# Performance work log

Measured on AMD Instinct MI355X. Metric: run time of the kernel, lower is better.

The kernel has to match this reference:

```python
import jax, jax.numpy as jnp
import numpy as np

DIM = 512
HEADS = 8
SCALE = (DIM / HEADS) ** (-0.5)  # = head_dim^-0.5


def setup_inputs() -> dict:
    key = jax.random.key(0)
    kq, kk, kv = jax.random.split(key, 3)
    B, N, D = 4, 2048, DIM
    return {
        "Q": jax.random.normal(kq, (B, N, D), dtype=jnp.float32),
        "K": jax.random.normal(kk, (B, N, D), dtype=jnp.float32),
        "V": jax.random.normal(kv, (B, N, D), dtype=jnp.float32),
    }


def _split_heads(x):
    b, n, hd = x.shape
    d = hd // HEADS
    return x.reshape(b, n, HEADS, d).transpose(0, 2, 1, 3)  # [b,h,n,d]


def reference(Q, K, V):
    q = _split_heads(Q)
    k = _split_heads(K)
    v = _split_heads(V)
    dots = jnp.einsum('bhid,bhjd->bhij', q, k) * SCALE
    attn = jax.nn.softmax(dots, axis=-1)
    out = jnp.einsum('bhij,bhjd->bhid', attn, v)
    b, h, n, d = out.shape
    return out.transpose(0, 2, 1, 3).reshape(b, n, h * d)
```

## Files before the change

### kernel.cpp

```cpp
#include <hip/hip_runtime.h>

typedef _Float16 half4 __attribute__((ext_vector_type(4)));
typedef _Float16 half8 __attribute__((ext_vector_type(8)));
typedef float floatx4 __attribute__((ext_vector_type(4)));

constexpr int NSEQ = 2048;
constexpr int NDIM = 512;
constexpr int DH   = 64;
constexpr float SCALE = 0.125f;
constexpr float SCALE_L2E = 0.125f * 1.44269504088896340736f;

constexpr int KB9 = 32;
constexpr int NT9 = NSEQ / KB9;
constexpr int KB = 64;
constexpr int NT = NSEQ / KB;

#if __has_builtin(__builtin_amdgcn_exp2f)
__device__ __forceinline__ float fast_exp2(float x) { return __builtin_amdgcn_exp2f(x); }
#else
__device__ __forceinline__ float fast_exp2(float x) {
    float r; asm("v_exp_f32 %0, %1\n\ts_nop 1" : "=v"(r) : "v"(x)); return r;
}
#endif

__global__ __launch_bounds__(256) void mha_prep9(const float* __restrict__ K,
                                                 const float* __restrict__ V,
                                                 _Float16* __restrict__ Kh,
                                                 _Float16* __restrict__ Vh)
{
    const int bid = blockIdx.x;
    const int isV = bid >> 11;
    const int t   = bid & 2047;
    const int kt  = t & 63, bh = t >> 6;
    const int h = bh & 7, b = bh >> 3;
    const int n0 = kt * KB9;
    _Float16* dst = (isV ? Vh : Kh) + (size_t)(bh * 64 + kt) * 2048;

    const int tid = threadIdx.x;
    const int f = tid >> 6, l = tid & 63, lr = l & 15, lg = l >> 4;
    half8 w;
    if (!isV) {
        const int row = n0 + (f >> 1) * 16 + lr;
        const int c0  = (f & 1) * 32 + lg * 8;
        const float* src = K + ((size_t)b * NSEQ + row) * NDIM + h * DH + c0;
        floatx4 x0 = *(const floatx4*)src;
        floatx4 x1 = *(const floatx4*)(src + 4);
        #pragma unroll
        for (int j = 0; j < 4; ++j) { w[j] = (_Float16)x0[j]; w[4 + j] = (_Float16)x1[j]; }
    } else {
        const int d  = f * 16 + lr;
        const int k0 = lg * 4;
        const float* src = V + ((size_t)(b * NSEQ + n0 + k0)) * NDIM + h * DH + d;
        #pragma unroll
        for (int j = 0; j < 4; ++j) {
            w[j]     = (_Float16)src[(size_t)j * NDIM];
            w[4 + j] = (_Float16)src[(size_t)(16 + j) * NDIM];
        }
    }
    *(half8*)(dst + (size_t)tid * 8) = w;
}

__launch_bounds__(256, 3)
__global__ void mha_fwd13(const float* __restrict__ Q,
                          const _Float16* __restrict__ Kh,
                          const _Float16* __restrict__ Vh,
                          float* __restrict__ O)
{
    __shared__ float mrg[2][34][64];

    const int tid = threadIdx.x, wave = tid >> 6, lane = tid & 63;
    const int qgrp = wave & 1, khalf = wave >> 1;
    const int lr = lane & 15, lg = lane >> 4;

    const int bid = blockIdx.x;
    const int bh  = (bid & 7) + 8 * (bid >> 8);
    const int qw  = (bid >> 3) & 31;
    const int h = bh & 7, b = bh >> 3;
    const int qrow0 = qw * 64 + qgrp * 32;

    half8 aq[2][2];
    #pragma unroll
    for (int qs = 0; qs < 2; ++qs) {
        const float* qp = Q + ((size_t)b * NSEQ + qrow0 + qs * 16 + lr) * NDIM + h * DH;
        #pragma unroll
        for (int c = 0; c < 2; ++c) {
            floatx4 x0 = *(const floatx4*)(qp + c * 32 + lg * 8);
            floatx4 x1 = *(const floatx4*)(qp + c * 32 + lg * 8 + 4);
            #pragma unroll
            for (int j = 0; j < 4; ++j) {
                aq[qs][c][j]     = (_Float16)(x0[j] * SCALE_L2E);
                aq[qs][c][4 + j] = (_Float16)(x1[j] * SCALE_L2E);
            }
        }
    }

    const char* kbase = (const char*)Kh + (size_t)bh * 64 * 4096 + lane * 16;
    const char* vbase = (const char*)Vh + (size_t)bh * 64 * 4096 + lane * 16;

    floatx4 accT[4][2];
    floatx4 accL[2];
    #pragma unroll
    for (int dt = 0; dt < 4; ++dt)
        #pragma unroll
        for (int qs = 0; qs < 2; ++qs) accT[dt][qs] = (floatx4){0.f, 0.f, 0.f, 0.f};
    #pragma unroll
    for (int qs = 0; qs < 2; ++qs) accL[qs] = (floatx4){0.f, 0.f, 0.f, 0.f};
    const half8 ones8 = {(_Float16)1.f, (_Float16)1.f, (_Float16)1.f, (_Float16)1.f,
                         (_Float16)1.f, (_Float16)1.f, (_Float16)1.f, (_Float16)1.f};

    half8 kA[4], kB[4];

    const int kt0 = khalf * (NT9 / 2);
    const int ktL = kt0 + NT9 / 2 - 1;

    auto LK = [&](int kt, half8* d) {
        const char* p = kbase + (size_t)kt * 4096;
        d[0] = *(const half8*)(p);
        d[1] = *(const half8*)(p + 1024);
        d[2] = *(const half8*)(p + 2048);
        d[3] = *(const half8*)(p + 3072);
    };

    auto BODY = [&](int kt, half8* kC, half8* kN) {
        const char* vp = vbase + (size_t)kt * 4096;
        half8 vf0 = *(const half8*)(vp);
        half8 vf1 = *(const half8*)(vp + 1024);
        half8 vf2 = *(const half8*)(vp + 2048);
        half8 vf3 = *(const half8*)(vp + 3072);
        const int ktn = (kt < ktL) ? kt + 1 : kt;
        LK(ktn, kN);

        #pragma unroll
        for (int qs = 0; qs < 2; ++qs) {
            floatx4 s0 = (floatx4){0.f, 0.f, 0.f, 0.f};
            s0 = __builtin_amdgcn_mfma_f32_16x16x32_f16(kC[0], aq[qs][0], s0, 0, 0, 0);
            s0 = __builtin_amdgcn_mfma_f32_16x16x32_f16(kC[1], aq[qs][1], s0, 0, 0, 0);
            floatx4 s1 = (floatx4){0.f, 0.f, 0.f, 0.f};
            s1 = __builtin_amdgcn_mfma_f32_16x16x32_f16(kC[2], aq[qs][0], s1, 0, 0, 0);
            s1 = __builtin_amdgcn_mfma_f32_16x16x32_f16(kC[3], aq[qs][1], s1, 0, 0, 0);

            union { unsigned int u[4]; half8 h; } pw;
            {
                const float e0 = fast_exp2(s0[0]);
                const float e1 = fast_exp2(s0[1]);
                const float e2 = fast_exp2(s0[2]);
                const float e3 = fast_exp2(s0[3]);
                pw.u[0] = __builtin_bit_cast(unsigned int, __builtin_amdgcn_cvt_pkrtz(e0, e1));
                pw.u[1] = __builtin_bit_cast(unsigned int, __builtin_amdgcn_cvt_pkrtz(e2, e3));
            }
            {
                const float e0 = fast_exp2(s1[0]);
                const float e1 = fast_exp2(s1[1]);
                const float e2 = fast_exp2(s1[2]);
                const float e3 = fast_exp2(s1[3]);
                pw.u[2] = __builtin_bit_cast(unsigned int, __builtin_amdgcn_cvt_pkrtz(e0, e1));
                pw.u[3] = __builtin_bit_cast(unsigned int, __builtin_amdgcn_cvt_pkrtz(e2, e3));
            }
            const half8 pb8 = pw.h;

            __builtin_amdgcn_s_setprio(1);
            accL[qs] = __builtin_amdgcn_mfma_f32_16x16x32_f16(ones8, pb8, accL[qs], 0, 0, 0);
            accT[0][qs] = __builtin_amdgcn_mfma_f32_16x16x32_f16(vf0, pb8, accT[0][qs], 0, 0, 0);
            accT[1][qs] = __builtin_amdgcn_mfma_f32_16x16x32_f16(vf1, pb8, accT[1][qs], 0, 0, 0);
            accT[2][qs] = __builtin_amdgcn_mfma_f32_16x16x32_f16(vf2, pb8, accT[2][qs], 0, 0, 0);
            accT[3][qs] = __builtin_amdgcn_mfma_f32_16x16x32_f16(vf3, pb8, accT[3][qs], 0, 0, 0);
            __builtin_amdgcn_s_setprio(0);
        }
    };

    LK(kt0, kA);
    for (int it = 0; it < NT9 / 2; it += 2) {
        BODY(kt0 + it,     kA, kB);
        BODY(kt0 + it + 1, kB, kA);
    }

    __syncthreads();
    if (khalf == 1) {
        float (*m)[64] = mrg[qgrp];
        #pragma unroll
        for (int dt = 0; dt < 4; ++dt)
            #pragma unroll
            for (int qs = 0; qs < 2; ++qs)
                #pragma unroll
                for (int r = 0; r < 4; ++r)
                    m[dt * 8 + qs * 4 + r][lane] = accT[dt][qs][r];
        #pragma unroll
        for (int qs = 0; qs < 2; ++qs) m[32 + qs][lane] = accL[qs][0];
    }
    __syncthreads();
    if (khalf == 0) {
        float (*m)[64] = mrg[qgrp];
        #pragma unroll
        for (int qs = 0; qs < 2; ++qs) {
            const float inv = 1.0f / (accL[qs][0] + m[32 + qs][lane]);
            float* op = O + ((size_t)b * NSEQ + qrow0 + qs * 16 + lr) * NDIM + h * DH;
            #pragma unroll
            for (int dt = 0; dt < 4; ++dt) {
                floatx4 o;
                #pragma unroll
                for (int r = 0; r < 4; ++r)
                    o[r] = (accT[dt][qs][r] + m[dt * 8 + qs * 4 + r][lane]) * inv;
                *(floatx4*)(op + dt * 16 + lg * 4) = o;
            }
        }
    }
}

constexpr int QB2 = 64;
constexpr int LDK = DH + 8;
constexpr int LDV = KB + 8;

__launch_bounds__(256, 4)
__global__ void mha_fwd2(const float* __restrict__ Q,
                         const float* __restrict__ K,
                         const float* __restrict__ V,
                         float* __restrict__ O)
{
    __shared__ _Float16 sK[2][KB * LDK];
    __shared__ _Float16 sVT[2][DH * LDV];

    const int tid = threadIdx.x, wave = tid >> 6, lane = tid & 63;
    const int lr = lane & 15, lg = lane >> 4;
    const int bid = blockIdx.x;
    const int qt = bid & 31, bh = bid >> 5;
    const int h = bh & 7, b = bh >> 3;
    const int qrow0 = qt * QB2 + wave * 16;

    half8 aq[2];
    {
        const float* qp = Q + ((size_t)b * NSEQ + qrow0 + lr) * NDIM + h * DH;
        #pragma unroll
        for (int c = 0; c < 2; ++c) {
            floatx4 x0 = *(const floatx4*)(qp + c * 32 + lg * 8);
            floatx4 x1 = *(const floatx4*)(qp + c * 32 + lg * 8 + 4);
            #pragma unroll
            for (int j = 0; j < 4; ++j) {
                aq[c][j] = (_Float16)(x0[j] * SCALE);
                aq[c][4 + j] = (_Float16)(x1[j] * SCALE);
            }
        }
    }
    const int jk = tid >> 2, ck = (tid & 3) * 16;
    const int jv = (tid & 15) * 4, cv = (tid >> 4) * 4;
    const float* kbase = K + (size_t)b * NSEQ * NDIM + h * DH;
    const float* vbase = V + (size_t)b * NSEQ * NDIM + h * DH;

    floatx4 rk[4], rv[4];
    auto LOAD = [&](int kt) {
        const float* ks = kbase + (size_t)(kt * KB + jk) * NDIM + ck;
        #pragma unroll
        for (int q4 = 0; q4 < 4; ++q4) rk[q4] = *(const floatx4*)(ks + q4 * 4);
        const float* vs = vbase + (size_t)(kt * KB + jv) * NDIM + cv;
        #pragma unroll
        for (int i = 0; i < 4; ++i) rv[i] = *(const floatx4*)(vs + (size_t)i * NDIM);
    };
    auto WRITE = [&](int buf) {
        #pragma unroll
        for (int q4 = 0; q4 < 4; ++q4) {
            half4 w = { (_Float16)rk[q4][0], (_Float16)rk[q4][1],
                        (_Float16)rk[q4][2], (_Float16)rk[q4][3] };
            *(half4*)&sK[buf][jk * LDK + ck + q4 * 4] = w;
        }
        #pragma unroll
        for (int cc = 0; cc < 4; ++cc) {
            half4 w = { (_Float16)rv[0][cc], (_Float16)rv[1][cc],
                        (_Float16)rv[2][cc], (_Float16)rv[3][cc] };
            *(half4*)&sVT[buf][(cv + cc) * LDV + jv] = w;
        }
    };

    floatx4 accT[4];
    #pragma unroll
    for (int t = 0; t < 4; ++t) accT[t] = (floatx4){0.f, 0.f, 0.f, 0.f};
    float m_run = -1e30f, l_run = 0.f;

    LOAD(0);
    #pragma unroll 2
    for (int kt = 0; kt < NT; ++kt) {
        const int buf = kt & 1;
        WRITE(buf);
        if (kt + 1 < NT) LOAD(kt + 1);
        __syncthreads();

        floatx4 s[4];
        #pragma unroll
        for (int t = 0; t < 4; ++t) {
            half8 bk0 = *(const half8*)&sK[buf][(t * 16 + lr) * LDK + lg * 8];
            half8 bk1 = *(const half8*)&sK[buf][(t * 16 + lr) * LDK + 32 + lg * 8];
            floatx4 z = (floatx4){0.f, 0.f, 0.f, 0.f};
            z = __builtin_amdgcn_mfma_f32_16x16x32_f16(bk0, aq[0], z, 0, 0, 0);
            z = __builtin_amdgcn_mfma_f32_16x16x32_f16(bk1, aq[1], z, 0, 0, 0);
            s[t] = z;
        }
        float lm = s[0][0];
        #pragma unroll
        for (int t = 0; t < 4; ++t)
            #pragma unroll
            for (int r = 0; r < 4; ++r) lm = fmaxf(lm, s[t][r]);
        lm = fmaxf(lm, __shfl_xor(lm, 16, 64));
        lm = fmaxf(lm, __shfl_xor(lm, 32, 64));
        const float mn = fmaxf(m_run, lm);
        const float f = __expf(m_run - mn);
        m_run = mn;
        #pragma unroll
        for (int t = 0; t < 4; ++t)
            #pragma unroll
            for (int r = 0; r < 4; ++r) s[t][r] = __expf(s[t][r] - mn);
        float ls = 0.f;
        #pragma unroll
        for (int t = 0; t < 4; ++t) ls += (s[t][0] + s[t][1]) + (s[t][2] + s[t][3]);
        ls += __shfl_xor(ls, 16, 64);
        ls += __shfl_xor(ls, 32, 64);
        l_run = l_run * f + ls;
        #pragma unroll
        for (int dt = 0; dt < 4; ++dt)
            #pragma unroll
            for (int r = 0; r < 4; ++r) accT[dt][r] *= f;

        half4 pb[4];
        #pragma unroll
        for (int t = 0; t < 4; ++t) {
            half4 w = { (_Float16)s[t][0], (_Float16)s[t][1],
                        (_Float16)s[t][2], (_Float16)s[t][3] };
            pb[t] = w;
        }
        #pragma unroll
        for (int dt = 0; dt < 4; ++dt) {
            #pragma unroll
            for (int t = 0; t < 4; ++t) {
                half4 va = *(const half4*)&sVT[buf][(dt * 16 + lr) * LDV + t * 16 + lg * 4];
                accT[dt] = __builtin_amdgcn_mfma_f32_16x16x16f16(va, pb[t], accT[dt], 0, 0, 0);
            }
        }
    }
    const float inv = 1.0f / l_run;
    float* op = O + ((size_t)b * NSEQ + qrow0 + lr) * NDIM + h * DH;
    #pragma unroll
    for (int dt = 0; dt < 4; ++dt) {
        floatx4 o;
        #pragma unroll
        for (int r = 0; r < 4; ++r) o[r] = accT[dt][r] * inv;
        *(floatx4*)(op + dt * 16 + lg * 4) = o;
    }
}

extern "C" void kernel_launch(void* const* d_in, const int* in_sizes, int n_in,
                              void* d_out, int out_size, void* d_ws, size_t ws_size,
                              hipStream_t stream) {
    const float* Q = (const float*)d_in[0];
    const float* K = (const float*)d_in[1];
    const float* V = (const float*)d_in[2];
    float* O = (float*)d_out;

    const size_t need = (size_t)2 * 32 * 64 * 2048 * sizeof(_Float16);
    if (ws_size >= need) {
        _Float16* Kh = (_Float16*)d_ws;
        _Float16* Vh = Kh + (size_t)32 * 64 * 2048;
        hipLaunchKernelGGL(mha_prep9, dim3(4096), dim3(256), 0, stream, K, V, Kh, Vh);
        hipLaunchKernelGGL(mha_fwd13, dim3(1024), dim3(256), 0, stream, Q, Kh, Vh, O);
    } else {
        hipLaunchKernelGGL(mha_fwd2, dim3(1024), dim3(256), 0, stream, Q, K, V, O);
    }
}
```

Measured before the change: 59.73 us.

## Shrink key tile to 16 and use 16x16x16 MFMA for PV

Halves the key block per iteration from 32 to 16. Score computation now uses one 16x16x32 MFMA pair per query subtile, and the PV and row-sum products use 16x16x16 MFMAs on half4 fragments. The prep kernel is rewritten to emit the matching 16-key K and V tile layouts, and launch bounds rise to 4 waves per SIMD to cut register pressure and raise occupancy. The cost is twice as many loop iterations, smaller loads and lower-K MFMAs with less throughput each.

```diff
diff --git a/kernel.cpp b/kernel.cpp
--- a/kernel.cpp
+++ b/kernel.cpp
@@ -10,8 +10,8 @@
 constexpr float SCALE = 0.125f;
 constexpr float SCALE_L2E = 0.125f * 1.44269504088896340736f;
 
-constexpr int KB9 = 32;
-constexpr int NT9 = NSEQ / KB9;
+constexpr int KB14 = 16;
+constexpr int NT14 = NSEQ / KB14;
 constexpr int KB = 64;
 constexpr int NT = NSEQ / KB;
 
@@ -23,45 +23,49 @@
 }
 #endif
 
-__global__ __launch_bounds__(256) void mha_prep9(const float* __restrict__ K,
-                                                 const float* __restrict__ V,
-                                                 _Float16* __restrict__ Kh,
-                                                 _Float16* __restrict__ Vh)
+__global__ __launch_bounds__(256) void mha_prep14(const float* __restrict__ K,
+                                                  const float* __restrict__ V,
+                                                  _Float16* __restrict__ Kh,
+                                                  _Float16* __restrict__ Vh)
 {
     const int bid = blockIdx.x;
-    const int isV = bid >> 11;
-    const int t   = bid & 2047;
-    const int kt  = t & 63, bh = t >> 6;
+    const int isV = bid >> 10;
+    const int t   = bid & 1023;
+    const int kt4 = t & 31, bh = t >> 5;
     const int h = bh & 7, b = bh >> 3;
-    const int n0 = kt * KB9;
-    _Float16* dst = (isV ? Vh : Kh) + (size_t)(bh * 64 + kt) * 2048;
 
     const int tid = threadIdx.x;
-    const int f = tid >> 6, l = tid & 63, lr = l & 15, lg = l >> 4;
-    half8 w;
+    const int sub = tid >> 6, l = tid & 63, lr = l & 15, lg = l >> 4;
+    const int kt = kt4 * 4 + sub;
+    const int n0 = kt * KB14;
+
     if (!isV) {
-        const int row = n0 + (f >> 1) * 16 + lr;
-        const int c0  = (f & 1) * 32 + lg * 8;
-        const float* src = K + ((size_t)b * NSEQ + row) * NDIM + h * DH + c0;
-        floatx4 x0 = *(const floatx4*)src;
-        floatx4 x1 = *(const floatx4*)(src + 4);
-        #pragma unroll
-        for (int j = 0; j < 4; ++j) { w[j] = (_Float16)x0[j]; w[4 + j] = (_Float16)x1[j]; }
+        _Float16* dst = Kh + ((size_t)bh * NT14 + kt) * 1024;
+        #pragma unroll
+        for (int c = 0; c < 2; ++c) {
+            const float* src = K + ((size_t)b * NSEQ + n0 + lr) * NDIM + h * DH + c * 32 + lg * 8;
+            floatx4 x0 = *(const floatx4*)src;
+            floatx4 x1 = *(const floatx4*)(src + 4);
+            half8 w;
+            #pragma unroll
+            for (int j = 0; j < 4; ++j) { w[j] = (_Float16)x0[j]; w[4 + j] = (_Float16)x1[j]; }
+            *(half8*)(dst + c * 512 + l * 8) = w;
+        }
     } else {
-        const int d  = f * 16 + lr;
-        const int k0 = lg * 4;
-        const float* src = V + ((size_t)(b * NSEQ + n0 + k0)) * NDIM + h * DH + d;
-        #pragma unroll
-        for (int j = 0; j < 4; ++j) {
-            w[j]     = (_Float16)src[(size_t)j * NDIM];
-            w[4 + j] = (_Float16)src[(size_t)(16 + j) * NDIM];
-        }
-    }
-    *(half8*)(dst + (size_t)tid * 8) = w;
-}
-
-__launch_bounds__(256, 3)
-__global__ void mha_fwd13(const float* __restrict__ Q,
+        _Float16* dst = Vh + ((size_t)bh * NT14 + kt) * 1024;
+        #pragma unroll
+        for (int dt = 0; dt < 4; ++dt) {
+            const float* src = V + ((size_t)(b * NSEQ + n0 + lg * 4)) * NDIM + h * DH + dt * 16 + lr;
+            half4 w;
+            #pragma unroll
+            for (int j = 0; j < 4; ++j) w[j] = (_Float16)src[(size_t)j * NDIM];
+            *(half4*)(dst + dt * 256 + l * 4) = w;
+        }
+    }
+}
+
+__launch_bounds__(256, 4)
+__global__ void mha_fwd14(const float* __restrict__ Q,
                           const _Float16* __restrict__ Kh,
                           const _Float16* __restrict__ Vh,
                           float* __restrict__ O)
@@ -94,8 +98,8 @@
         }
     }
 
-    const char* kbase = (const char*)Kh + (size_t)bh * 64 * 4096 + lane * 16;
-    const char* vbase = (const char*)Vh + (size_t)bh * 64 * 4096 + lane * 16;
+    const char* kbase = (const char*)Kh + (size_t)bh * NT14 * 2048 + lane * 16;
+    const char* vbase = (const char*)Vh + (size_t)bh * NT14 * 2048 + lane * 8;
 
     floatx4 accT[4][2];
     floatx4 accL[2];
@@ -105,73 +109,64 @@
         for (int qs = 0; qs < 2; ++qs) accT[dt][qs] = (floatx4){0.f, 0.f, 0.f, 0.f};
     #pragma unroll
     for (int qs = 0; qs < 2; ++qs) accL[qs] = (floatx4){0.f, 0.f, 0.f, 0.f};
-    const half8 ones8 = {(_Float16)1.f, (_Float16)1.f, (_Float16)1.f, (_Float16)1.f,
-                         (_Float16)1.f, (_Float16)1.f, (_Float16)1.f, (_Float16)1.f};
-
-    half8 kA[4], kB[4];
-
-    const int kt0 = khalf * (NT9 / 2);
-    const int ktL = kt0 + NT9 / 2 - 1;
+    const half4 ones4 = {(_Float16)1.f, (_Float16)1.f, (_Float16)1.f, (_Float16)1.f};
+
+    half8 kA[2], kB[2];
+    half4 vA[4], vB[4];
+
+    const int kt0 = khalf * (NT14 / 2);
+    const int ktL = kt0 + NT14 / 2 - 1;
 
     auto LK = [&](int kt, half8* d) {
-        const char* p = kbase + (size_t)kt * 4096;
+        const char* p = kbase + (size_t)kt * 2048;
         d[0] = *(const half8*)(p);
         d[1] = *(const half8*)(p + 1024);
-        d[2] = *(const half8*)(p + 2048);
-        d[3] = *(const half8*)(p + 3072);
-    };
-
-    auto BODY = [&](int kt, half8* kC, half8* kN) {
-        const char* vp = vbase + (size_t)kt * 4096;
-        half8 vf0 = *(const half8*)(vp);
-        half8 vf1 = *(const half8*)(vp + 1024);
-        half8 vf2 = *(const half8*)(vp + 2048);
-        half8 vf3 = *(const half8*)(vp + 3072);
+    };
+    auto LV = [&](int kt, half4* d) {
+        const char* p = vbase + (size_t)kt * 2048;
+        d[0] = *(const half4*)(p);
+        d[1] = *(const half4*)(p + 512);
+        d[2] = *(const half4*)(p + 1024);
+        d[3] = *(const half4*)(p + 1536);
+    };
+
+    auto BODY = [&](int kt, half8* kC, half4* vC, half8* kN, half4* vN) {
         const int ktn = (kt < ktL) ? kt + 1 : kt;
         LK(ktn, kN);
+        LV(ktn, vN);
 
         #pragma unroll
         for (int qs = 0; qs < 2; ++qs) {
-            floatx4 s0 = (floatx4){0.f, 0.f, 0.f, 0.f};
-            s0 = __builtin_amdgcn_mfma_f32_16x16x32_f16(kC[0], aq[qs][0], s0, 0, 0, 0);
-            s0 = __builtin_amdgcn_mfma_f32_16x16x32_f16(kC[1], aq[qs][1], s0, 0, 0, 0);
-            floatx4 s1 = (floatx4){0.f, 0.f, 0.f, 0.f};
-            s1 = __builtin_amdgcn_mfma_f32_16x16x32_f16(kC[2], aq[qs][0], s1, 0, 0, 0);
-            s1 = __builtin_amdgcn_mfma_f32_16x16x32_f16(kC[3], aq[qs][1], s1, 0, 0, 0);
-
-            union { unsigned int u[4]; half8 h; } pw;
+            floatx4 s = (floatx4){0.f, 0.f, 0.f, 0.f};
+            s = __builtin_amdgcn_mfma_f32_16x16x32_f16(kC[0], aq[qs][0], s, 0, 0, 0);
+            s = __builtin_amdgcn_mfma_f32_16x16x32_f16(kC[1], aq[qs][1], s, 0, 0, 0);
+
+            union { unsigned int u[2]; half4 h; } pw;
             {
-                const float e0 = fast_exp2(s0[0]);
-                const float e1 = fast_exp2(s0[1]);
-                const float e2 = fast_exp2(s0[2]);
-                const float e3 = fast_exp2(s0[3]);
+                const float e0 = fast_exp2(s[0]);
+                const float e1 = fast_exp2(s[1]);
+                const float e2 = fast_exp2(s[2]);
+                const float e3 = fast_exp2(s[3]);
                 pw.u[0] = __builtin_bit_cast(unsigned int, __builtin_amdgcn_cvt_pkrtz(e0, e1));
                 pw.u[1] = __builtin_bit_cast(unsigned int, __builtin_amdgcn_cvt_pkrtz(e2, e3));
             }
-            {
-                const float e0 = fast_exp2(s1[0]);
-                const float e1 = fast_exp2(s1[1]);
-                const float e2 = fast_exp2(s1[2]);
-                const float e3 = fast_exp2(s1[3]);
-                pw.u[2] = __builtin_bit_cast(unsigned int, __builtin_amdgcn_cvt_pkrtz(e0, e1));
-                pw.u[3] = __builtin_bit_cast(unsigned int, __builtin_amdgcn_cvt_pkrtz(e2, e3));
-            }
-            const half8 pb8 = pw.h;
+            const half4 pb = pw.h;
 
             __builtin_amdgcn_s_setprio(1);
-            accL[qs] = __builtin_amdgcn_mfma_f32_16x16x32_f16(ones8, pb8, accL[qs], 0, 0, 0);
-            accT[0][qs] = __builtin_amdgcn_mfma_f32_16x16x32_f16(vf0, pb8, accT[0][qs], 0, 0, 0);
-            accT[1][qs] = __builtin_amdgcn_mfma_f32_16x16x32_f16(vf1, pb8, accT[1][qs], 0, 0, 0);
-            accT[2][qs] = __builtin_amdgcn_mfma_f32_16x16x32_f16(vf2, pb8, accT[2][qs], 0, 0, 0);
-            accT[3][qs] = __builtin_amdgcn_mfma_f32_16x16x32_f16(vf3, pb8, accT[3][qs], 0, 0, 0);
+            accL[qs] = __builtin_amdgcn_mfma_f32_16x16x16f16(ones4, pb, accL[qs], 0, 0, 0);
+            accT[0][qs] = __builtin_amdgcn_mfma_f32_16x16x16f16(vC[0], pb, accT[0][qs], 0, 0, 0);
+            accT[1][qs] = __builtin_amdgcn_mfma_f32_16x16x16f16(vC[1], pb, accT[1][qs], 0, 0, 0);
+            accT[2][qs] = __builtin_amdgcn_mfma_f32_16x16x16f16(vC[2], pb, accT[2][qs], 0, 0, 0);
+            accT[3][qs] = __builtin_amdgcn_mfma_f32_16x16x16f16(vC[3], pb, accT[3][qs], 0, 0, 0);
             __builtin_amdgcn_s_setprio(0);
         }
     };
 
     LK(kt0, kA);
-    for (int it = 0; it < NT9 / 2; it += 2) {
-        BODY(kt0 + it,     kA, kB);
-        BODY(kt0 + it + 1, kB, kA);
+    LV(kt0, vA);
+    for (int it = 0; it < NT14 / 2; it += 2) {
+        BODY(kt0 + it,     kA, vA, kB, vB);
+        BODY(kt0 + it + 1, kB, vB, kA, vA);
     }
 
     __syncthreads();
@@ -352,12 +347,12 @@
     const float* V = (const float*)d_in[2];
     float* O = (float*)d_out;
 
-    const size_t need = (size_t)2 * 32 * 64 * 2048 * sizeof(_Float16);
+    const size_t need = (size_t)2 * 32 * NT14 * 1024 * sizeof(_Float16);
     if (ws_size >= need) {
         _Float16* Kh = (_Float16*)d_ws;
-        _Float16* Vh = Kh + (size_t)32 * 64 * 2048;
-        hipLaunchKernelGGL(mha_prep9, dim3(4096), dim3(256), 0, stream, K, V, Kh, Vh);
-        hipLaunchKernelGGL(mha_fwd13, dim3(1024), dim3(256), 0, stream, Q, Kh, Vh, O);
+        _Float16* Vh = Kh + (size_t)32 * NT14 * 1024;
+        hipLaunchKernelGGL(mha_prep14, dim3(2048), dim3(256), 0, stream, K, V, Kh, Vh);
+        hipLaunchKernelGGL(mha_fwd14, dim3(1024), dim3(256), 0, stream, Q, Kh, Vh, O);
     } else {
         hipLaunchKernelGGL(mha_fwd2, dim3(1024), dim3(256), 0, stream, Q, K, V, O);
     }
```

Measured after the change: 69.19 us. +15.8%, slower.
